# Kernel optimization log

Hardware: AMD Instinct MI355X
Metric: run time of the kernel (lower is better)

Reference implementation:

```python
import jax, jax.numpy as jnp
import numpy as np

N_STATE = 64   # n == m (required by the broadcast in the original forward)
SEQ_LEN = 200000


def setup_inputs() -> dict:
    key = jax.random.key(0)
    k_y, k_a, k_h = jax.random.split(key, 3)
    n = N_STATE
    # A scaled so spectral radius ~0.9 (stable recurrence), H ~ O(1) rows
    A = 0.9 * jax.random.normal(k_a, (n, n), dtype=jnp.float32) / jnp.sqrt(jnp.float32(n))
    H = jax.random.normal(k_h, (n, n), dtype=jnp.float32) / jnp.sqrt(jnp.float32(n))
    y = jax.random.normal(k_y, (n, SEQ_LEN), dtype=jnp.float32)
    L = jnp.float32(0.2)  # scalar learned gain (self.weights)
    return {"y": y, "A": A, "H": H, "L": L, "N": SEQ_LEN}


def reference(y, A, H, L, N):
    # x_{k+1} = A x_k + L * (y_k - H x_k);  yhat_k = H x_k  (pre-update state)
    # Vectorized over time with lax.scan (true sequential dependence).
    def step(x, yk):
        out = H @ x                      # [n] observation prediction at step k
        x_next = A @ x + L * (yk - out)  # [n] state update
        return x_next, out

    x0 = jnp.zeros((A.shape[0],), dtype=y.dtype)
    _, yhat_t = jax.lax.scan(step, x0, y.T)  # scan over time axis: y.T is [N, m]
    return yhat_t.T                          # [m, N]
```

## Files before the change

kernel.cpp:

```cpp
#include <hip/hip_runtime.h>


#define CHUNK 64
#define LOOKBACK 8

__device__ __forceinline__ float bcast(float x, int l) {
  return __uint_as_float(__builtin_amdgcn_readlane(__float_as_uint(x), l));
}

__global__ __launch_bounds__(1024) void kf_setup(const float* __restrict__ A,
                                                 const float* __restrict__ Hm,
                                                 const float* __restrict__ Lp,
                                                 float* __restrict__ ws) {
  __shared__ __align__(16) float s0[64 * 68];
  __shared__ __align__(16) float s1[64 * 68];
  const float Lg = Lp[0];
  const int t  = threadIdx.x;
  const int r  = t >> 4;
  const int c0 = (t & 15) * 4;

  if (t < 512) ws[4096 + t] = 0.f;

  {
    const float4 a4 = *(const float4*)(A  + r * 64 + c0);
    const float4 h4 = *(const float4*)(Hm + r * 64 + c0);
    float4 m4;
    m4.x = fmaf(-Lg, h4.x, a4.x);
    m4.y = fmaf(-Lg, h4.y, a4.y);
    m4.z = fmaf(-Lg, h4.z, a4.z);
    m4.w = fmaf(-Lg, h4.w, a4.w);
    *(float4*)(s0 + r * 68 + c0) = m4;
  }
  __syncthreads();

  float* src = s0;
  float* dst = s1;
  for (int sq = 0; sq < 6; ++sq) {
    float4 acc = make_float4(0.f, 0.f, 0.f, 0.f);
    const float* srow = src + r * 68;
    #pragma unroll 8
    for (int k = 0; k < 64; ++k) {
      const float  a  = srow[k];
      const float4 b4 = *(const float4*)(src + k * 68 + c0);
      acc.x = fmaf(a, b4.x, acc.x);
      acc.y = fmaf(a, b4.y, acc.y);
      acc.z = fmaf(a, b4.z, acc.z);
      acc.w = fmaf(a, b4.w, acc.w);
    }
    __syncthreads();
    *(float4*)(dst + r * 68 + c0) = acc;
    __syncthreads();
    float* tmp = src; src = dst; dst = tmp;
  }
  *(float4*)(ws + r * 64 + c0) = *(const float4*)(src + r * 68 + c0);
}

__global__ __launch_bounds__(64, 2) void kf_phase1(const float* __restrict__ y,
                                                   const float* __restrict__ A,
                                                   const float* __restrict__ Hm,
                                                   const float* __restrict__ Lp,
                                                   float* __restrict__ bb,
                                                   int Nv, int P) {
  const int lane = threadIdx.x;
  const float Lg = Lp[0];
  const int c0 = min(2 * (int)blockIdx.x,     P - 1);
  const int c1 = min(2 * (int)blockIdx.x + 1, P - 1);

  float Mrow[64];
  {
    const float* Ar = A  + lane * 64;
    const float* Hr = Hm + lane * 64;
    #pragma unroll
    for (int j = 0; j < 64; j += 4) {
      const float4 a4 = *(const float4*)(Ar + j);
      const float4 h4 = *(const float4*)(Hr + j);
      Mrow[j + 0] = fmaf(-Lg, h4.x, a4.x);
      Mrow[j + 1] = fmaf(-Lg, h4.y, a4.y);
      Mrow[j + 2] = fmaf(-Lg, h4.z, a4.z);
      Mrow[j + 3] = fmaf(-Lg, h4.w, a4.w);
    }
  }

  const float* yr0 = y + (size_t)lane * (size_t)Nv + c0 * CHUNK;
  const float* yr1 = y + (size_t)lane * (size_t)Nv + c1 * CHUNK;
  float x0 = 0.f, x1 = 0.f;

  #pragma unroll 1
  for (int t = 0; t < 8; ++t) {
    const float4 pa0 = *(const float4*)(yr0 + 8 * t);
    const float4 pb0 = *(const float4*)(yr0 + 8 * t + 4);
    const float4 pa1 = *(const float4*)(yr1 + 8 * t);
    const float4 pb1 = *(const float4*)(yr1 + 8 * t + 4);
    const float yb0[8] = {pa0.x, pa0.y, pa0.z, pa0.w, pb0.x, pb0.y, pb0.z, pb0.w};
    const float yb1[8] = {pa1.x, pa1.y, pa1.z, pa1.w, pb1.x, pb1.y, pb1.z, pb1.w};
    #pragma unroll
    for (int kk = 0; kk < 8; ++kk) {
      float a0 = 0.f, a1 = 0.f, b0 = 0.f, b1 = 0.f;
      #pragma unroll
      for (int j = 0; j < 64; j += 2) {
        const float s0 = bcast(x0, j);
        const float s1 = bcast(x1, j);
        const float u0 = bcast(x0, j + 1);
        const float u1 = bcast(x1, j + 1);
        a0 = fmaf(Mrow[j],     s0, a0);
        b0 = fmaf(Mrow[j],     s1, b0);
        a1 = fmaf(Mrow[j + 1], u0, a1);
        b1 = fmaf(Mrow[j + 1], u1, b1);
      }
      x0 = fmaf(Lg, yb0[kk], a0 + a1);
      x1 = fmaf(Lg, yb1[kk], b0 + b1);
    }
  }
  bb[c0 * 64 + lane] = x0;
  bb[c1 * 64 + lane] = x1;
}

__global__ __launch_bounds__(64, 1) void kf_phase3(const float* __restrict__ y,
                                                   const float* __restrict__ A,
                                                   const float* __restrict__ Hm,
                                                   const float* __restrict__ Lp,
                                                   const float* __restrict__ bb,
                                                   const float* __restrict__ P64,
                                                   float* __restrict__ out,
                                                   int Nv, int P) {
  const int lane = threadIdx.x;
  const float Lg = Lp[0];
  const int c0 = min(2 * (int)blockIdx.x,     P - 1);
  const int c1 = min(2 * (int)blockIdx.x + 1, P - 1);

  float Mrow[64];
  {
    const float* Ar = A  + lane * 64;
    const float* Hr = Hm + lane * 64;
    #pragma unroll
    for (int j = 0; j < 64; j += 4) {
      const float4 a4 = *(const float4*)(Ar + j);
      const float4 h4 = *(const float4*)(Hr + j);
      Mrow[j + 0] = fmaf(-Lg, h4.x, a4.x);
      Mrow[j + 1] = fmaf(-Lg, h4.y, a4.y);
      Mrow[j + 2] = fmaf(-Lg, h4.z, a4.z);
      Mrow[j + 3] = fmaf(-Lg, h4.w, a4.w);
    }
  }

  float x0, x1;
  {
    float Prow[64];
    #pragma unroll
    for (int j = 0; j < 64; j += 4) {
      const float4 p4 = *(const float4*)(P64 + lane * 64 + j);
      Prow[j + 0] = p4.x; Prow[j + 1] = p4.y;
      Prow[j + 2] = p4.z; Prow[j + 3] = p4.w;
    }
    x0 = bb[(c0 - LOOKBACK) * 64 + lane];
    x1 = bb[(c1 - LOOKBACK) * 64 + lane];
    #pragma unroll 1
    for (int t = LOOKBACK - 1; t >= 1; --t) {
      float a0 = 0.f, a1 = 0.f, b0 = 0.f, b1 = 0.f;
      #pragma unroll
      for (int j = 0; j < 64; j += 2) {
        const float s0 = bcast(x0, j);
        const float s1 = bcast(x1, j);
        const float u0 = bcast(x0, j + 1);
        const float u1 = bcast(x1, j + 1);
        a0 = fmaf(Prow[j],     s0, a0);
        b0 = fmaf(Prow[j],     s1, b0);
        a1 = fmaf(Prow[j + 1], u0, a1);
        b1 = fmaf(Prow[j + 1], u1, b1);
      }
      x0 = (a0 + a1) + bb[(c0 - t) * 64 + lane];
      x1 = (b0 + b1) + bb[(c1 - t) * 64 + lane];
    }
  }

  float Hrow[64];
  #pragma unroll
  for (int j = 0; j < 64; j += 4) {
    const float4 h4 = *(const float4*)(Hm + lane * 64 + j);
    Hrow[j + 0] = h4.x; Hrow[j + 1] = h4.y;
    Hrow[j + 2] = h4.z; Hrow[j + 3] = h4.w;
  }

  const float* yr0 = y   + (size_t)lane * (size_t)Nv + c0 * CHUNK;
  const float* yr1 = y   + (size_t)lane * (size_t)Nv + c1 * CHUNK;
  float*       o0  = out + (size_t)lane * (size_t)Nv + c0 * CHUNK;
  float*       o1  = out + (size_t)lane * (size_t)Nv + c1 * CHUNK;

  #pragma unroll 1
  for (int t = 0; t < 8; ++t) {
    const float4 pa0 = *(const float4*)(yr0 + 8 * t);
    const float4 pb0 = *(const float4*)(yr0 + 8 * t + 4);
    const float4 pa1 = *(const float4*)(yr1 + 8 * t);
    const float4 pb1 = *(const float4*)(yr1 + 8 * t + 4);
    const float yb0[8] = {pa0.x, pa0.y, pa0.z, pa0.w, pb0.x, pb0.y, pb0.z, pb0.w};
    const float yb1[8] = {pa1.x, pa1.y, pa1.z, pa1.w, pb1.x, pb1.y, pb1.z, pb1.w};
    float ob0[8], ob1[8];

    #pragma unroll
    for (int kk = 0; kk < 8; ++kk) {
      float h0a = 0.f, h0b = 0.f, m0a = 0.f, m0b = 0.f;
      float h1a = 0.f, h1b = 0.f, m1a = 0.f, m1b = 0.f;
      #pragma unroll
      for (int j = 0; j < 64; j += 2) {
        const float s0 = bcast(x0, j);
        const float s1 = bcast(x1, j);
        const float u0 = bcast(x0, j + 1);
        const float u1 = bcast(x1, j + 1);
        h0a = fmaf(Hrow[j],     s0, h0a);
        m0a = fmaf(Mrow[j],     s0, m0a);
        h1a = fmaf(Hrow[j],     s1, h1a);
        m1a = fmaf(Mrow[j],     s1, m1a);
        h0b = fmaf(Hrow[j + 1], u0, h0b);
        m0b = fmaf(Mrow[j + 1], u0, m0b);
        h1b = fmaf(Hrow[j + 1], u1, h1b);
        m1b = fmaf(Mrow[j + 1], u1, m1b);
      }
      ob0[kk] = h0a + h0b;
      ob1[kk] = h1a + h1b;
      x0 = fmaf(Lg, yb0[kk], m0a + m0b);
      x1 = fmaf(Lg, yb1[kk], m1a + m1b);
    }
    *(float4*)(o0 + 8 * t)     = make_float4(ob0[0], ob0[1], ob0[2], ob0[3]);
    *(float4*)(o0 + 8 * t + 4) = make_float4(ob0[4], ob0[5], ob0[6], ob0[7]);
    *(float4*)(o1 + 8 * t)     = make_float4(ob1[0], ob1[1], ob1[2], ob1[3]);
    *(float4*)(o1 + 8 * t + 4) = make_float4(ob1[4], ob1[5], ob1[6], ob1[7]);
  }
}

extern "C" void kernel_launch(void* const* d_in, const int* in_sizes, int n_in,
                              void* d_out, int out_size, void* d_ws, size_t ws_size,
                              hipStream_t stream) {
  const float* y  = (const float*)d_in[0];
  const float* A  = (const float*)d_in[1];
  const float* Hm = (const float*)d_in[2];
  const float* Lp = (const float*)d_in[3];
  const int Nv = in_sizes[0] / 64;
  const int P  = (Nv + CHUNK - 1) / CHUNK;
  const int B2 = (P + 1) / 2;

  float* ws   = (float*)d_ws;
  float* P64  = ws;
  float* bb   = ws + 4096 + 512;

  kf_setup<<<1, 1024, 0, stream>>>(A, Hm, Lp, ws);
  kf_phase1<<<B2, 64, 0, stream>>>(y, A, Hm, Lp, bb, Nv, P);
  kf_phase3<<<B2, 64, 0, stream>>>(y, A, Hm, Lp, bb, P64, (float*)d_out, Nv, P);
}
```

Baseline: 318.7 us.

## Split H projection out of the sequential scan into a parallel GEMM kernel

The second recurrence pass now only advances the state with M = A - L·H and stores each pre-update state into the output buffer. A new kernel then computes H·x in place, one column per lane, fully in parallel. This takes the H dot products off the serial dependency chain, at the cost of an extra read and write pass over the 64×N output. Separately, phase 1 now runs four independent chunk recurrences per wavefront instead of two, to get more instruction-level parallelism per broadcast. The GEMM kernel assumes N is a multiple of 64 and has no bounds check.

```diff
diff --git a/kernel.cpp b/kernel.cpp
--- a/kernel.cpp
+++ b/kernel.cpp
@@ -63,8 +63,10 @@
                                                    int Nv, int P) {
   const int lane = threadIdx.x;
   const float Lg = Lp[0];
-  const int c0 = min(2 * (int)blockIdx.x,     P - 1);
-  const int c1 = min(2 * (int)blockIdx.x + 1, P - 1);
+  const int c0 = min(4 * (int)blockIdx.x + 0, P - 1);
+  const int c1 = min(4 * (int)blockIdx.x + 1, P - 1);
+  const int c2 = min(4 * (int)blockIdx.x + 2, P - 1);
+  const int c3 = min(4 * (int)blockIdx.x + 3, P - 1);
 
   float Mrow[64];
   {
@@ -83,7 +85,9 @@
 
   const float* yr0 = y + (size_t)lane * (size_t)Nv + c0 * CHUNK;
   const float* yr1 = y + (size_t)lane * (size_t)Nv + c1 * CHUNK;
-  float x0 = 0.f, x1 = 0.f;
+  const float* yr2 = y + (size_t)lane * (size_t)Nv + c2 * CHUNK;
+  const float* yr3 = y + (size_t)lane * (size_t)Nv + c3 * CHUNK;
+  float x0 = 0.f, x1 = 0.f, x2 = 0.f, x3 = 0.f;
 
   #pragma unroll 1
   for (int t = 0; t < 8; ++t) {
@@ -91,38 +95,48 @@
     const float4 pb0 = *(const float4*)(yr0 + 8 * t + 4);
     const float4 pa1 = *(const float4*)(yr1 + 8 * t);
     const float4 pb1 = *(const float4*)(yr1 + 8 * t + 4);
+    const float4 pa2 = *(const float4*)(yr2 + 8 * t);
+    const float4 pb2 = *(const float4*)(yr2 + 8 * t + 4);
+    const float4 pa3 = *(const float4*)(yr3 + 8 * t);
+    const float4 pb3 = *(const float4*)(yr3 + 8 * t + 4);
     const float yb0[8] = {pa0.x, pa0.y, pa0.z, pa0.w, pb0.x, pb0.y, pb0.z, pb0.w};
     const float yb1[8] = {pa1.x, pa1.y, pa1.z, pa1.w, pb1.x, pb1.y, pb1.z, pb1.w};
+    const float yb2[8] = {pa2.x, pa2.y, pa2.z, pa2.w, pb2.x, pb2.y, pb2.z, pb2.w};
+    const float yb3[8] = {pa3.x, pa3.y, pa3.z, pa3.w, pb3.x, pb3.y, pb3.z, pb3.w};
     #pragma unroll
     for (int kk = 0; kk < 8; ++kk) {
-      float a0 = 0.f, a1 = 0.f, b0 = 0.f, b1 = 0.f;
+      float a0 = 0.f, a1 = 0.f, a2 = 0.f, a3 = 0.f;
       #pragma unroll
-      for (int j = 0; j < 64; j += 2) {
+      for (int j = 0; j < 64; ++j) {
         const float s0 = bcast(x0, j);
         const float s1 = bcast(x1, j);
-        const float u0 = bcast(x0, j + 1);
-        const float u1 = bcast(x1, j + 1);
-        a0 = fmaf(Mrow[j],     s0, a0);
-        b0 = fmaf(Mrow[j],     s1, b0);
-        a1 = fmaf(Mrow[j + 1], u0, a1);
-        b1 = fmaf(Mrow[j + 1], u1, b1);
+        const float s2 = bcast(x2, j);
+        const float s3 = bcast(x3, j);
+        a0 = fmaf(Mrow[j], s0, a0);
+        a1 = fmaf(Mrow[j], s1, a1);
+        a2 = fmaf(Mrow[j], s2, a2);
+        a3 = fmaf(Mrow[j], s3, a3);
       }
-      x0 = fmaf(Lg, yb0[kk], a0 + a1);
-      x1 = fmaf(Lg, yb1[kk], b0 + b1);
+      x0 = fmaf(Lg, yb0[kk], a0);
+      x1 = fmaf(Lg, yb1[kk], a1);
+      x2 = fmaf(Lg, yb2[kk], a2);
+      x3 = fmaf(Lg, yb3[kk], a3);
     }
   }
   bb[c0 * 64 + lane] = x0;
   bb[c1 * 64 + lane] = x1;
-}
-
-__global__ __launch_bounds__(64, 1) void kf_phase3(const float* __restrict__ y,
-                                                   const float* __restrict__ A,
-                                                   const float* __restrict__ Hm,
-                                                   const float* __restrict__ Lp,
-                                                   const float* __restrict__ bb,
-                                                   const float* __restrict__ P64,
-                                                   float* __restrict__ out,
-                                                   int Nv, int P) {
+  bb[c2 * 64 + lane] = x2;
+  bb[c3 * 64 + lane] = x3;
+}
+
+__global__ __launch_bounds__(64, 2) void kf_scan2(const float* __restrict__ y,
+                                                  const float* __restrict__ A,
+                                                  const float* __restrict__ Hm,
+                                                  const float* __restrict__ Lp,
+                                                  const float* __restrict__ bb,
+                                                  const float* __restrict__ P64,
+                                                  float* __restrict__ X,
+                                                  int Nv, int P) {
   const int lane = threadIdx.x;
   const float Lg = Lp[0];
   const int c0 = min(2 * (int)blockIdx.x,     P - 1);
@@ -173,18 +187,10 @@
     }
   }
 
-  float Hrow[64];
-  #pragma unroll
-  for (int j = 0; j < 64; j += 4) {
-    const float4 h4 = *(const float4*)(Hm + lane * 64 + j);
-    Hrow[j + 0] = h4.x; Hrow[j + 1] = h4.y;
-    Hrow[j + 2] = h4.z; Hrow[j + 3] = h4.w;
-  }
-
-  const float* yr0 = y   + (size_t)lane * (size_t)Nv + c0 * CHUNK;
-  const float* yr1 = y   + (size_t)lane * (size_t)Nv + c1 * CHUNK;
-  float*       o0  = out + (size_t)lane * (size_t)Nv + c0 * CHUNK;
-  float*       o1  = out + (size_t)lane * (size_t)Nv + c1 * CHUNK;
+  const float* yr0 = y + (size_t)lane * (size_t)Nv + c0 * CHUNK;
+  const float* yr1 = y + (size_t)lane * (size_t)Nv + c1 * CHUNK;
+  float*       X0  = X + (size_t)lane * (size_t)Nv + c0 * CHUNK;
+  float*       X1  = X + (size_t)lane * (size_t)Nv + c1 * CHUNK;
 
   #pragma unroll 1
   for (int t = 0; t < 8; ++t) {
@@ -194,36 +200,55 @@
     const float4 pb1 = *(const float4*)(yr1 + 8 * t + 4);
     const float yb0[8] = {pa0.x, pa0.y, pa0.z, pa0.w, pb0.x, pb0.y, pb0.z, pb0.w};
     const float yb1[8] = {pa1.x, pa1.y, pa1.z, pa1.w, pb1.x, pb1.y, pb1.z, pb1.w};
-    float ob0[8], ob1[8];
+    float xb0[8], xb1[8];
 
     #pragma unroll
     for (int kk = 0; kk < 8; ++kk) {
-      float h0a = 0.f, h0b = 0.f, m0a = 0.f, m0b = 0.f;
-      float h1a = 0.f, h1b = 0.f, m1a = 0.f, m1b = 0.f;
+      xb0[kk] = x0;
+      xb1[kk] = x1;
+      float a0 = 0.f, a1 = 0.f, b0 = 0.f, b1 = 0.f;
       #pragma unroll
       for (int j = 0; j < 64; j += 2) {
         const float s0 = bcast(x0, j);
         const float s1 = bcast(x1, j);
         const float u0 = bcast(x0, j + 1);
         const float u1 = bcast(x1, j + 1);
-        h0a = fmaf(Hrow[j],     s0, h0a);
-        m0a = fmaf(Mrow[j],     s0, m0a);
-        h1a = fmaf(Hrow[j],     s1, h1a);
-        m1a = fmaf(Mrow[j],     s1, m1a);
-        h0b = fmaf(Hrow[j + 1], u0, h0b);
-        m0b = fmaf(Mrow[j + 1], u0, m0b);
-        h1b = fmaf(Hrow[j + 1], u1, h1b);
-        m1b = fmaf(Mrow[j + 1], u1, m1b);
+        a0 = fmaf(Mrow[j],     s0, a0);
+        b0 = fmaf(Mrow[j],     s1, b0);
+        a1 = fmaf(Mrow[j + 1], u0, a1);
+        b1 = fmaf(Mrow[j + 1], u1, b1);
       }
-      ob0[kk] = h0a + h0b;
-      ob1[kk] = h1a + h1b;
-      x0 = fmaf(Lg, yb0[kk], m0a + m0b);
-      x1 = fmaf(Lg, yb1[kk], m1a + m1b);
-    }
-    *(float4*)(o0 + 8 * t)     = make_float4(ob0[0], ob0[1], ob0[2], ob0[3]);
-    *(float4*)(o0 + 8 * t + 4) = make_float4(ob0[4], ob0[5], ob0[6], ob0[7]);
-    *(float4*)(o1 + 8 * t)     = make_float4(ob1[0], ob1[1], ob1[2], ob1[3]);
-    *(float4*)(o1 + 8 * t + 4) = make_float4(ob1[4], ob1[5], ob1[6], ob1[7]);
+      x0 = fmaf(Lg, yb0[kk], a0 + a1);
+      x1 = fmaf(Lg, yb1[kk], b0 + b1);
+    }
+    *(float4*)(X0 + 8 * t)     = make_float4(xb0[0], xb0[1], xb0[2], xb0[3]);
+    *(float4*)(X0 + 8 * t + 4) = make_float4(xb0[4], xb0[5], xb0[6], xb0[7]);
+    *(float4*)(X1 + 8 * t)     = make_float4(xb1[0], xb1[1], xb1[2], xb1[3]);
+    *(float4*)(X1 + 8 * t + 4) = make_float4(xb1[4], xb1[5], xb1[6], xb1[7]);
+  }
+}
+
+__global__ __launch_bounds__(64, 4) void kf_hgemm(const float* __restrict__ Hm,
+                                                  float* xo, int Nv) {
+  const int lane = threadIdx.x;
+  const int k    = (int)blockIdx.x * CHUNK + lane;
+
+  float xcol[64];
+  #pragma unroll
+  for (int r = 0; r < 64; ++r) {
+    xcol[r] = xo[(size_t)r * (size_t)Nv + k];
+  }
+
+  #pragma unroll 1
+  for (int r = 0; r < 64; ++r) {
+    const float* hr = Hm + r * 64;
+    float a0 = 0.f, a1 = 0.f;
+    #pragma unroll
+    for (int j = 0; j < 64; j += 2) {
+      a0 = fmaf(hr[j],     xcol[j],     a0);
+      a1 = fmaf(hr[j + 1], xcol[j + 1], a1);
+    }
+    xo[(size_t)r * (size_t)Nv + k] = a0 + a1;
   }
 }
 
@@ -236,13 +261,13 @@
   const float* Lp = (const float*)d_in[3];
   const int Nv = in_sizes[0] / 64;
   const int P  = (Nv + CHUNK - 1) / CHUNK;
-  const int B2 = (P + 1) / 2;
 
   float* ws   = (float*)d_ws;
   float* P64  = ws;
   float* bb   = ws + 4096 + 512;
 
   kf_setup<<<1, 1024, 0, stream>>>(A, Hm, Lp, ws);
-  kf_phase1<<<B2, 64, 0, stream>>>(y, A, Hm, Lp, bb, Nv, P);
-  kf_phase3<<<B2, 64, 0, stream>>>(y, A, Hm, Lp, bb, P64, (float*)d_out, Nv, P);
-}
+  kf_phase1<<<(P + 3) / 4, 64, 0, stream>>>(y, A, Hm, Lp, bb, Nv, P);
+  kf_scan2<<<(P + 1) / 2, 64, 0, stream>>>(y, A, Hm, Lp, bb, P64, (float*)d_out, Nv, P);
+  kf_hgemm<<<P, 64, 0, stream>>>(Hm, (float*)d_out, Nv);
+}
```

New measurement: 279.9 us. 1.14x faster.
